# Kernel optimization log

Hardware: AMD Instinct MI355X
Metric: run time of the kernel (lower is better)

The kernel has to match this reference:

```python
import jax, jax.numpy as jnp
import numpy as np

N = 100000   # num_nodes
E = 1600000  # num_edges
R = 8        # num_rels
B = 4        # num_bases
D = 64       # inp_dim = h_dim = out_dim


def setup_inputs() -> dict:
    key = jax.random.key(0)
    ks = jax.random.split(key, 16)
    s = 1.0 / np.sqrt(D)
    inp = {
        'h': jax.random.normal(ks[0], (N, D), jnp.float32),
        'src': jax.random.randint(ks[1], (E,), 0, N),
        'dst': jax.random.randint(ks[2], (E,), 0, N),
        'etype': jax.random.randint(ks[3], (E,), 0, R),
        'norm': jax.random.uniform(ks[4], (E, 1), jnp.float32),
    }
    for i in range(3):  # i2h, hidden, h2o layers (basis decomposition)
        inp[f'bases{i}'] = jax.random.normal(ks[5 + 2 * i], (B, D, D), jnp.float32) * s
        inp[f'wcomp{i}'] = jax.random.normal(ks[6 + 2 * i], (R, B), jnp.float32) * s
    inp['dec_w1'] = jax.random.normal(ks[11], (D, D), jnp.float32) * s
    inp['dec_b1'] = jnp.zeros((D,), jnp.float32)
    inp['dec_w2'] = jax.random.normal(ks[12], (D, 1), jnp.float32) * s
    inp['dec_b2'] = jnp.zeros((1,), jnp.float32)
    return inp


def rgcn_layer(h, src, dst, etype, norm, bases, wcomp, activate):
    # basis decomposition: W_r = sum_b wcomp[r,b] * bases[b]
    W = jnp.einsum('rb,bio->rio', wcomp, bases)           # [R, D, D]
    # transform all nodes under every relation (dense GEMM), then gather per edge
    Ht = jnp.einsum('ni,rio->rno', h, W).reshape(R * N, -1)  # [R*N, D]
    msg = Ht[etype * N + src] * norm                      # [E, D] gather + norm
    out = jax.ops.segment_sum(msg, dst, num_segments=N)   # scatter-add to dst
    return jax.nn.relu(out) if activate else out


def reference(h, src, dst, etype, norm, bases0, wcomp0, bases1, wcomp1,
              bases2, wcomp2, dec_w1, dec_b1, dec_w2, dec_b2):
    # EncoderRGCN: i2h (relu) -> hidden (relu) -> h2o (no activation)
    h1 = rgcn_layer(h, src, dst, etype, norm, bases0, wcomp0, True)
    h2 = rgcn_layer(h1, src, dst, etype, norm, bases1, wcomp1, True)
    henc = rgcn_layer(h2, src, dst, etype, norm, bases2, wcomp2, False)
    # AttributeDecoder: Linear -> ReLU -> Linear(reconstruct_dim=1)
    d1 = jax.nn.relu(henc @ dec_w1 + dec_b1)
    rec = (d1 @ dec_w2 + dec_b2).squeeze()                # [N]
    return rec, henc
```

## Files before the change

kernel.cpp:

```cpp
#include <hip/hip_runtime.h>

typedef _Float16 half8 __attribute__((ext_vector_type(8)));
typedef _Float16 half4 __attribute__((ext_vector_type(4)));
typedef _Float16 half2v __attribute__((ext_vector_type(2)));
typedef float floatx4 __attribute__((ext_vector_type(4)));

constexpr int NN = 100000;
constexpr int EE = 1600000;
constexpr int NBK = 196;
constexpr int CHUNK = 6250;
constexpr int CAPB = 12288;
constexpr int NDCAP = 40;

__global__ __launch_bounds__(256) void k_part(const int* __restrict__ dst,
                                              const int* __restrict__ src,
                                              const int* __restrict__ etype,
                                              const float* __restrict__ norm,
                                              int* __restrict__ gcur,
                                              int2* __restrict__ part) {
  __shared__ int2 ldata[CHUNK];
  __shared__ unsigned char lbkt[CHUNK];
  __shared__ int lhist[NBK], lbase[NBK + 1], lcur[NBK], gbase[NBK];
  __shared__ int sh[256];
  const int tid = threadIdx.x;
  const int e0 = blockIdx.x * CHUNK;

  for (int b = tid; b < NBK; b += 256) lhist[b] = 0;
  __syncthreads();
  for (int i = tid; i < CHUNK; i += 256)
    atomicAdd(&lhist[dst[e0 + i] >> 9], 1);
  __syncthreads();
  {
    const int v = (tid < NBK) ? lhist[tid] : 0;
    sh[tid] = v;
    __syncthreads();
    int run = v;
    for (int d = 1; d < 256; d <<= 1) {
      int t = (tid >= d) ? sh[tid - d] : 0;
      __syncthreads();
      run += t;
      sh[tid] = run;
      __syncthreads();
    }
    if (tid < NBK) {
      lbase[tid] = run - v;
      lcur[tid] = 0;
      gbase[tid] = tid * CAPB + atomicAdd(&gcur[tid], v);
    }
    if (tid == 0) lbase[NBK] = CHUNK;
  }
  __syncthreads();
  for (int i = tid; i < CHUNK; i += 256) {
    const int e = e0 + i;
    const int d = dst[e], s = src[e], et = etype[e];
    const _Float16 nh = (_Float16)norm[e];
    const unsigned short n16 = __builtin_bit_cast(unsigned short, nh);
    const int bk = d >> 9;
    const int pos = lbase[bk] + atomicAdd(&lcur[bk], 1);
    ldata[pos] = make_int2((d << 15) | (s >> 2), (s & 3) | (et << 2) | ((int)n16 << 5));
    lbkt[pos] = (unsigned char)bk;
  }
  __syncthreads();
  for (int i = tid; i < CHUNK; i += 256) {
    const int bk = (int)lbkt[i];
    part[gbase[bk] + (i - lbase[bk])] = ldata[i];
  }
}

__global__ __launch_bounds__(256) void k_scanB(const int* __restrict__ gcur,
                                               int* __restrict__ ebase) {
  __shared__ int wsum[4];
  const int tid = threadIdx.x;
  const int v = (tid < NBK) ? gcur[tid] : 0;
  int incl = v;
  for (int d = 1; d < 64; d <<= 1) {
    const int t = __shfl_up(incl, d);
    if ((tid & 63) >= d) incl += t;
  }
  if ((tid & 63) == 63) wsum[tid >> 6] = incl;
  __syncthreads();
  int add = 0;
  for (int w = 0; w < (tid >> 6); ++w) add += wsum[w];
  incl += add;
  if (tid < NBK) ebase[tid] = incl - v;
  if (tid == NBK - 1) ebase[NBK] = incl;
}

__global__ __launch_bounds__(256) void k_part2(const int* __restrict__ gcur,
                                               const int* __restrict__ ebase,
                                               const int2* __restrict__ part,
                                               int* __restrict__ off,
                                               int2* __restrict__ em) {
  __shared__ int hcnt[512];
  __shared__ int obase[512];
  __shared__ int sh[256];
  const int tid = threadIdx.x;
  const int bk = blockIdx.x;
  const int nb0 = bk << 9;
  const int cntb = gcur[bk];
  const int base = ebase[bk];
  const int2* __restrict__ pp = part + (size_t)bk * CAPB;

  hcnt[tid] = 0;
  hcnt[tid + 256] = 0;
  __syncthreads();
  for (int i = tid; i < cntb; i += 256)
    atomicAdd(&hcnt[(((unsigned)pp[i].x) >> 15) & 511], 1);
  __syncthreads();
  const int c0 = hcnt[2 * tid], c1 = hcnt[2 * tid + 1];
  const int psum = c0 + c1;
  sh[tid] = psum;
  __syncthreads();
  int run = psum;
  for (int d = 1; d < 256; d <<= 1) {
    int t = (tid >= d) ? sh[tid - d] : 0;
    __syncthreads();
    run += t;
    sh[tid] = run;
    __syncthreads();
  }
  const int excl = run - psum;
  obase[2 * tid] = excl;
  obase[2 * tid + 1] = excl + c0;
  __syncthreads();
  {
    const int n = nb0 + tid;
    if (n < NN) off[n] = base + obase[tid];
    const int n2 = nb0 + 256 + tid;
    if (n2 < NN) off[n2] = base + obase[256 + tid];
  }
  if (bk == NBK - 1 && tid == 0) off[NN] = EE;
  hcnt[tid] = obase[tid];
  hcnt[tid + 256] = obase[tid + 256];
  __syncthreads();
  for (int i = tid; i < cntb; i += 256) {
    const int2 r = pp[i];
    const int d = ((unsigned)r.x) >> 15;
    const int s = ((r.x & 0x7FFF) << 2) | (r.y & 3);
    const int et = (r.y >> 2) & 7;
    const unsigned short n16 = (unsigned short)((r.y >> 5) & 0xFFFF);
    const float nf = (float)__builtin_bit_cast(_Float16, n16);
    const int pos = atomicAdd(&hcnt[d & 511], 1);
    em[base + pos] = make_int2((et << 20) | s, __float_as_int(nf));
  }
}


__global__ __launch_bounds__(256) void k_prep(const float* __restrict__ h,
                                              _Float16* __restrict__ hh,
                                              const float* __restrict__ b0,
                                              const float* __restrict__ b1,
                                              const float* __restrict__ b2,
                                              _Float16* __restrict__ bbt) {
  const int bx = blockIdx.x;
  if (bx < 6250) {
    const int i = bx * 256 + threadIdx.x;
    const float4 v = *(const float4*)&h[(size_t)i * 4];
    half4 o = {(_Float16)v.x, (_Float16)v.y, (_Float16)v.z, (_Float16)v.w};
    *(half4*)&hh[(size_t)i * 4] = o;
  } else {
    const int g = (bx - 6250) >> 6;
    const int idx = ((bx - 6250) & 63) * 256 + threadIdx.x;
    const float* bases = (g == 0) ? b0 : (g == 1) ? b1 : b2;
    const int o = idx >> 8, k = idx & 255;
    const int b = k >> 6, i = k & 63;
    bbt[g * 16384 + idx] = (_Float16)bases[b * 4096 + i * 64 + o];
  }
}

__global__ __launch_bounds__(256, 8) void k_layer(const _Float16* __restrict__ hh,
                                                  const int* __restrict__ off,
                                                  const int2* __restrict__ em,
                                                  const float* __restrict__ wcomp,
                                                  const _Float16* __restrict__ bbt,
                                                  _Float16* __restrict__ out16,
                                                  float* __restrict__ out32) {
  __shared__ _Float16 Ash[16 * 264];
  __shared__ int4 ems[16 * NDCAP];
  __shared__ float4 wcs[8];
  __shared__ int offs[17];
  __shared__ int ovf;
  const int tid = threadIdx.x;
  const int lane = tid & 63;
  const int wv = tid >> 6;
  const int n0 = blockIdx.x * 16;

  if (tid < 17) offs[tid] = off[n0 + tid];
  if (tid == 0) ovf = 0;
  if (tid < 8) wcs[tid] = ((const float4*)wcomp)[tid];
  for (int i = tid; i < 16 * NDCAP; i += 256) ems[i] = make_int4(0, 0, 0, 0);
  __syncthreads();

  const int e0 = offs[0];
  const int len = offs[16] - e0;
  for (int i = tid; i < len; i += 256) {
    const int g = e0 + i;
    const int2 r = em[g];
    int lo = 0, hi = 15;
    while (lo < hi) { const int mid = (lo + hi + 1) >> 1; if (offs[mid] <= g) lo = mid; else hi = mid - 1; }
    const int rank = g - offs[lo];
    const int et = r.x >> 20;
    const int s = r.x & 0xFFFFF;
    const float nf = __int_as_float(r.y);
    const float4 w = wcs[et];
    half2v c01 = {(_Float16)(nf * w.x), (_Float16)(nf * w.y)};
    half2v c23 = {(_Float16)(nf * w.z), (_Float16)(nf * w.w)};
    if (rank < NDCAP)
      ems[lo * NDCAP + rank] = make_int4(s, __builtin_bit_cast(int, c01),
                                         __builtin_bit_cast(int, c23), 0);
    else ovf = 1;
  }
  __syncthreads();

  if (!ovf) {
    const int fl = lane & 31;
    const int eg = lane >> 5;
    const half2v* __restrict__ hp = (const half2v*)hh;
    for (int q = 0; q < 4; ++q) {
      const int m = wv * 4 + q;
      const int cnt = offs[m + 1] - offs[m];
      const int nbat = (cnt + 7) >> 3;
      const int4* ep = &ems[m * NDCAP + eg * 4];
      float a0 = 0.f, a1 = 0.f, a2 = 0.f, a3 = 0.f;
      float a4 = 0.f, a5 = 0.f, a6 = 0.f, a7 = 0.f;
      for (int b = 0; b < nbat; ++b) {
        int4 rr[4];
#pragma unroll
        for (int j = 0; j < 4; ++j) rr[j] = ep[b * 8 + j];
        half2v hv[4];
#pragma unroll
        for (int j = 0; j < 4; ++j)
          hv[j] = hp[(unsigned)rr[j].x * 32u + fl];
#pragma unroll
        for (int j = 0; j < 4; ++j) {
          const half2v c01 = __builtin_bit_cast(half2v, rr[j].y);
          const half2v c23 = __builtin_bit_cast(half2v, rr[j].z);
          const float h0 = (float)hv[j][0], h1 = (float)hv[j][1];
          a0 = fmaf(h0, (float)c01[0], a0); a1 = fmaf(h1, (float)c01[0], a1);
          a2 = fmaf(h0, (float)c01[1], a2); a3 = fmaf(h1, (float)c01[1], a3);
          a4 = fmaf(h0, (float)c23[0], a4); a5 = fmaf(h1, (float)c23[0], a5);
          a6 = fmaf(h0, (float)c23[1], a6); a7 = fmaf(h1, (float)c23[1], a7);
        }
      }
      a0 += __shfl_xor(a0, 32); a1 += __shfl_xor(a1, 32);
      a2 += __shfl_xor(a2, 32); a3 += __shfl_xor(a3, 32);
      a4 += __shfl_xor(a4, 32); a5 += __shfl_xor(a5, 32);
      a6 += __shfl_xor(a6, 32); a7 += __shfl_xor(a7, 32);
      if (eg == 0) {
        _Float16* ar = &Ash[m * 264];
        *(half2v*)&ar[0 * 64 + 2 * fl] = half2v{(_Float16)a0, (_Float16)a1};
        *(half2v*)&ar[1 * 64 + 2 * fl] = half2v{(_Float16)a2, (_Float16)a3};
        *(half2v*)&ar[2 * 64 + 2 * fl] = half2v{(_Float16)a4, (_Float16)a5};
        *(half2v*)&ar[3 * 64 + 2 * fl] = half2v{(_Float16)a6, (_Float16)a7};
      }
    }
  } else {
    const _Float16* hl = hh + lane;
    for (int q = 0; q < 4; ++q) {
      const int m = wv * 4 + q;
      const int p0 = offs[m], p1 = offs[m + 1];
      float a0 = 0.f, a1 = 0.f, a2 = 0.f, a3 = 0.f;
      for (int p = p0; p < p1; p += 8) {
#pragma unroll
        for (int j = 0; j < 8; ++j) {
          const bool live = (p + j < p1);
          const int idx = live ? p + j : p1 - 1;
          const int2 mm = em[idx];
          const float hv = (float)hl[(size_t)(mm.x & 0xFFFFF) << 6];
          const float wn = live ? __int_as_float(mm.y) : 0.f;
          const float4 w = wcs[mm.x >> 20];
          const float t = wn * hv;
          a0 = fmaf(t, w.x, a0); a1 = fmaf(t, w.y, a1);
          a2 = fmaf(t, w.z, a2); a3 = fmaf(t, w.w, a3);
        }
      }
      _Float16* ar = &Ash[m * 264];
      ar[lane]       = (_Float16)a0;
      ar[64 + lane]  = (_Float16)a1;
      ar[128 + lane] = (_Float16)a2;
      ar[192 + lane] = (_Float16)a3;
    }
  }
  __syncthreads();

  const int col = lane & 15;
  const int quad = lane >> 4;
  const int obase = wv * 16 + col;
  const _Float16* ap = &Ash[col * 264 + quad * 8];
  const _Float16* bp = &bbt[(size_t)obase * 256 + quad * 8];
  floatx4 acc = {0.f, 0.f, 0.f, 0.f};
#pragma unroll
  for (int s = 0; s < 8; ++s) {
    const half8 af = *(const half8*)(ap + s * 32);
    const half8 bf = *(const half8*)(bp + s * 32);
    acc = __builtin_amdgcn_mfma_f32_16x16x32_f16(af, bf, acc, 0, 0, 0);
  }
  if (out16) {
#pragma unroll
    for (int r = 0; r < 4; ++r) {
      const float c = fmaxf(acc[r], 0.f);
      out16[(size_t)(n0 + quad * 4 + r) * 64 + obase] = (_Float16)c;
    }
  } else {
#pragma unroll
    for (int r = 0; r < 4; ++r) {
      out32[(size_t)(n0 + quad * 4 + r) * 64 + obase] = acc[r];
    }
  }
}

__global__ __launch_bounds__(256) void k_dec(const float* __restrict__ henc,
                                             const float* __restrict__ w1,
                                             const float* __restrict__ b1,
                                             const float* __restrict__ w2,
                                             const float* __restrict__ b2,
                                             float* __restrict__ rec) {
  __shared__ float w1s[64 * 64];
  __shared__ float hs[16 * 68];
  const int tid = threadIdx.x;
  for (int r = tid; r < 1024; r += 256)
    *(float4*)&w1s[r * 4] = *(const float4*)&w1[r * 4];
  const int og = tid & 15;
  const int nl = tid >> 4;
  const float4 wv2 = *(const float4*)&w2[og * 4];
  const float4 bv1 = *(const float4*)&b1[og * 4];
  const float b2v = b2[0];
  for (int t0 = blockIdx.x * 16; t0 < NN; t0 += gridDim.x * 16) {
    __syncthreads();
    {
      const float4 hv = *(const float4*)&henc[(size_t)t0 * 64 + tid * 4];
      *(float4*)&hs[(tid >> 4) * 68 + (tid & 15) * 4] = hv;
    }
    __syncthreads();
    float4 acc = bv1;
    const float* hr = &hs[nl * 68];
#pragma unroll 8
    for (int i = 0; i < 64; ++i) {
      const float hv = hr[i];
      const float4 wv = *(const float4*)&w1s[i * 64 + og * 4];
      acc.x = fmaf(hv, wv.x, acc.x); acc.y = fmaf(hv, wv.y, acc.y);
      acc.z = fmaf(hv, wv.z, acc.z); acc.w = fmaf(hv, wv.w, acc.w);
    }
    acc.x = fmaxf(acc.x, 0.f); acc.y = fmaxf(acc.y, 0.f);
    acc.z = fmaxf(acc.z, 0.f); acc.w = fmaxf(acc.w, 0.f);
    float v = acc.x * wv2.x + acc.y * wv2.y + acc.z * wv2.z + acc.w * wv2.w;
    v += __shfl_xor(v, 1); v += __shfl_xor(v, 2);
    v += __shfl_xor(v, 4); v += __shfl_xor(v, 8);
    if (og == 0) rec[t0 + nl] = v + b2v;
  }
}


extern "C" void kernel_launch(void* const* d_in, const int* in_sizes, int n_in,
                              void* d_out, int out_size, void* d_ws, size_t ws_size,
                              hipStream_t stream) {
  const float* h     = (const float*)d_in[0];
  const int*   src   = (const int*)d_in[1];
  const int*   dst   = (const int*)d_in[2];
  const int*   etype = (const int*)d_in[3];
  const float* norm  = (const float*)d_in[4];
  const float* bases[3] = {(const float*)d_in[5], (const float*)d_in[7], (const float*)d_in[9]};
  const float* wcomp[3] = {(const float*)d_in[6], (const float*)d_in[8], (const float*)d_in[10]};
  const float* dw1 = (const float*)d_in[11];
  const float* db1 = (const float*)d_in[12];
  const float* dw2 = (const float*)d_in[13];
  const float* db2 = (const float*)d_in[14];

  float* rec  = (float*)d_out;
  float* henc = (float*)d_out + NN;

  char* ws = (char*)d_ws;
  int*      off    = (int*)(ws + 0);
  int*      gcur   = (int*)(ws + 400512);
  int*      ebase  = (int*)(ws + 401536);
  int2*     em     = (int2*)(ws + 402560);
  _Float16* hh     = (_Float16*)(ws + 13202560);
  _Float16* h1f    = (_Float16*)(ws + 26002560);
  _Float16* h2f    = (_Float16*)(ws + 38802560);
  _Float16* bbt    = (_Float16*)(ws + 51602560);
  int2*     part   = (int2*)h1f;

  k_prep<<<6250 + 192, 256, 0, stream>>>(h, hh, bases[0], bases[1], bases[2], bbt);

  hipMemsetAsync(gcur, 0, NBK * sizeof(int), stream);
  k_part<<<256, 256, 0, stream>>>(dst, src, etype, norm, gcur, part);
  k_scanB<<<1, 256, 0, stream>>>(gcur, ebase);
  k_part2<<<NBK, 256, 0, stream>>>(gcur, ebase, part, off, em);

  k_layer<<<NN / 16, 256, 0, stream>>>(hh,  off, em, wcomp[0], bbt,         h1f, nullptr);
  k_layer<<<NN / 16, 256, 0, stream>>>(h1f, off, em, wcomp[1], bbt + 16384, h2f, nullptr);
  k_layer<<<NN / 16, 256, 0, stream>>>(h2f, off, em, wcomp[2], bbt + 32768, nullptr, henc);

  k_dec<<<256, 256, 0, stream>>>(henc, dw1, db1, dw2, db2, rec);
}
```

Measured before the change: 379.7 us.

## Pack fp16 aggregation, merge bucket scan into part2, fold memset into prep

The per-edge aggregation in the layer kernel now accumulates in packed half2 arithmetic, with source indices and broadcast coefficient pairs held in separate shared arrays and 8 edges per batch. The bucket-offset scan kernel is removed: each part2 block reduces the preceding bucket counts itself and uses 512 threads for its in-bucket scan. The gcur memset moves into the prep kernel, and partitioning uses smaller chunks across more blocks. NDCAP is raised and the occupancy hint lowered. Accumulating in fp16 cuts ALU work and conversions but risks precision loss, and the larger shared memory footprint may reduce occupancy.

Result: faster. 360.5 us (-5.1%).

```diff
diff --git a/kernel.cpp b/kernel.cpp
--- a/kernel.cpp
+++ b/kernel.cpp
@@ -8,9 +8,9 @@
 constexpr int NN = 100000;
 constexpr int EE = 1600000;
 constexpr int NBK = 196;
-constexpr int CHUNK = 6250;
+constexpr int CHUNK = 3125;
 constexpr int CAPB = 12288;
-constexpr int NDCAP = 40;
+constexpr int NDCAP = 48;
 
 __global__ __launch_bounds__(256) void k_part(const int* __restrict__ dst,
                                               const int* __restrict__ src,
@@ -67,73 +67,52 @@
   }
 }
 
-__global__ __launch_bounds__(256) void k_scanB(const int* __restrict__ gcur,
-                                               int* __restrict__ ebase) {
-  __shared__ int wsum[4];
+__global__ __launch_bounds__(512) void k_part2(const int* __restrict__ gcur,
+                                               const int2* __restrict__ part,
+                                               int* __restrict__ off,
+                                               int2* __restrict__ em) {
+  __shared__ int hcnt[512];
+  __shared__ int wred[8];
+  __shared__ int swsum[8];
   const int tid = threadIdx.x;
-  const int v = (tid < NBK) ? gcur[tid] : 0;
+  const int bk = blockIdx.x;
+  const int nb0 = bk << 9;
+  const int2* __restrict__ pp = part + (size_t)bk * CAPB;
+
+  {
+    int pv = (tid < bk) ? gcur[tid] : 0;
+    for (int d = 32; d > 0; d >>= 1) pv += __shfl_down(pv, d);
+    if ((tid & 63) == 0) wred[tid >> 6] = pv;
+  }
+  hcnt[tid] = 0;
+  __syncthreads();
+  int base = 0;
+#pragma unroll
+  for (int w = 0; w < 8; ++w) base += wred[w];
+  const int cntb = gcur[bk];
+
+  for (int i = tid; i < cntb; i += 512)
+    atomicAdd(&hcnt[(((unsigned)pp[i].x) >> 15) & 511], 1);
+  __syncthreads();
+  const int v = hcnt[tid];
   int incl = v;
   for (int d = 1; d < 64; d <<= 1) {
     const int t = __shfl_up(incl, d);
     if ((tid & 63) >= d) incl += t;
   }
-  if ((tid & 63) == 63) wsum[tid >> 6] = incl;
-  __syncthreads();
-  int add = 0;
-  for (int w = 0; w < (tid >> 6); ++w) add += wsum[w];
-  incl += add;
-  if (tid < NBK) ebase[tid] = incl - v;
-  if (tid == NBK - 1) ebase[NBK] = incl;
-}
-
-__global__ __launch_bounds__(256) void k_part2(const int* __restrict__ gcur,
-                                               const int* __restrict__ ebase,
-                                               const int2* __restrict__ part,
-                                               int* __restrict__ off,
-                                               int2* __restrict__ em) {
-  __shared__ int hcnt[512];
-  __shared__ int obase[512];
-  __shared__ int sh[256];
-  const int tid = threadIdx.x;
-  const int bk = blockIdx.x;
-  const int nb0 = bk << 9;
-  const int cntb = gcur[bk];
-  const int base = ebase[bk];
-  const int2* __restrict__ pp = part + (size_t)bk * CAPB;
-
-  hcnt[tid] = 0;
-  hcnt[tid + 256] = 0;
-  __syncthreads();
-  for (int i = tid; i < cntb; i += 256)
-    atomicAdd(&hcnt[(((unsigned)pp[i].x) >> 15) & 511], 1);
-  __syncthreads();
-  const int c0 = hcnt[2 * tid], c1 = hcnt[2 * tid + 1];
-  const int psum = c0 + c1;
-  sh[tid] = psum;
-  __syncthreads();
-  int run = psum;
-  for (int d = 1; d < 256; d <<= 1) {
-    int t = (tid >= d) ? sh[tid - d] : 0;
-    __syncthreads();
-    run += t;
-    sh[tid] = run;
-    __syncthreads();
-  }
-  const int excl = run - psum;
-  obase[2 * tid] = excl;
-  obase[2 * tid + 1] = excl + c0;
-  __syncthreads();
+  if ((tid & 63) == 63) swsum[tid >> 6] = incl;
+  __syncthreads();
+  int pre = 0;
+  for (int w = 0; w < (tid >> 6); ++w) pre += swsum[w];
+  const int excl = pre + incl - v;
   {
     const int n = nb0 + tid;
-    if (n < NN) off[n] = base + obase[tid];
-    const int n2 = nb0 + 256 + tid;
-    if (n2 < NN) off[n2] = base + obase[256 + tid];
+    if (n < NN) off[n] = base + excl;
   }
   if (bk == NBK - 1 && tid == 0) off[NN] = EE;
-  hcnt[tid] = obase[tid];
-  hcnt[tid + 256] = obase[tid + 256];
-  __syncthreads();
-  for (int i = tid; i < cntb; i += 256) {
+  hcnt[tid] = excl;
+  __syncthreads();
+  for (int i = tid; i < cntb; i += 512) {
     const int2 r = pp[i];
     const int d = ((unsigned)r.x) >> 15;
     const int s = ((r.x & 0x7FFF) << 2) | (r.y & 3);
@@ -151,8 +130,10 @@
                                               const float* __restrict__ b0,
                                               const float* __restrict__ b1,
                                               const float* __restrict__ b2,
-                                              _Float16* __restrict__ bbt) {
+                                              _Float16* __restrict__ bbt,
+                                              int* __restrict__ gcur) {
   const int bx = blockIdx.x;
+  if (bx == 0 && threadIdx.x < NBK) gcur[threadIdx.x] = 0;
   if (bx < 6250) {
     const int i = bx * 256 + threadIdx.x;
     const float4 v = *(const float4*)&h[(size_t)i * 4];
@@ -168,7 +149,7 @@
   }
 }
 
-__global__ __launch_bounds__(256, 8) void k_layer(const _Float16* __restrict__ hh,
+__global__ __launch_bounds__(256, 6) void k_layer(const _Float16* __restrict__ hh,
                                                   const int* __restrict__ off,
                                                   const int2* __restrict__ em,
                                                   const float* __restrict__ wcomp,
@@ -176,7 +157,8 @@
                                                   _Float16* __restrict__ out16,
                                                   float* __restrict__ out32) {
   __shared__ _Float16 Ash[16 * 264];
-  __shared__ int4 ems[16 * NDCAP];
+  __shared__ int  ems_s[16 * NDCAP];
+  __shared__ int4 ems_c[16 * NDCAP];
   __shared__ float4 wcs[8];
   __shared__ int offs[17];
   __shared__ int ovf;
@@ -188,7 +170,10 @@
   if (tid < 17) offs[tid] = off[n0 + tid];
   if (tid == 0) ovf = 0;
   if (tid < 8) wcs[tid] = ((const float4*)wcomp)[tid];
-  for (int i = tid; i < 16 * NDCAP; i += 256) ems[i] = make_int4(0, 0, 0, 0);
+  for (int i = tid; i < 16 * NDCAP; i += 256) {
+    ems_s[i] = 0;
+    ems_c[i] = make_int4(0, 0, 0, 0);
+  }
   __syncthreads();
 
   const int e0 = offs[0];
@@ -203,12 +188,15 @@
     const int s = r.x & 0xFFFFF;
     const float nf = __int_as_float(r.y);
     const float4 w = wcs[et];
-    half2v c01 = {(_Float16)(nf * w.x), (_Float16)(nf * w.y)};
-    half2v c23 = {(_Float16)(nf * w.z), (_Float16)(nf * w.w)};
-    if (rank < NDCAP)
-      ems[lo * NDCAP + rank] = make_int4(s, __builtin_bit_cast(int, c01),
-                                         __builtin_bit_cast(int, c23), 0);
-    else ovf = 1;
+    const _Float16 c0 = (_Float16)(nf * w.x), c1 = (_Float16)(nf * w.y);
+    const _Float16 c2 = (_Float16)(nf * w.z), c3 = (_Float16)(nf * w.w);
+    const half2v p0 = {c0, c0}, p1 = {c1, c1}, p2 = {c2, c2}, p3 = {c3, c3};
+    if (rank < NDCAP) {
+      ems_s[lo * NDCAP + rank] = s;
+      ems_c[lo * NDCAP + rank] = make_int4(
+          __builtin_bit_cast(int, p0), __builtin_bit_cast(int, p1),
+          __builtin_bit_cast(int, p2), __builtin_bit_cast(int, p3));
+    } else ovf = 1;
   }
   __syncthreads();
 
@@ -219,39 +207,37 @@
     for (int q = 0; q < 4; ++q) {
       const int m = wv * 4 + q;
       const int cnt = offs[m + 1] - offs[m];
-      const int nbat = (cnt + 7) >> 3;
-      const int4* ep = &ems[m * NDCAP + eg * 4];
-      float a0 = 0.f, a1 = 0.f, a2 = 0.f, a3 = 0.f;
-      float a4 = 0.f, a5 = 0.f, a6 = 0.f, a7 = 0.f;
+      const int nbat = (cnt + 15) >> 4;
+      const int* sp = &ems_s[m * NDCAP + eg * 8];
+      const int4* cp = &ems_c[m * NDCAP + eg * 8];
+      half2v a0 = {0, 0}, a1 = {0, 0}, a2 = {0, 0}, a3 = {0, 0};
       for (int b = 0; b < nbat; ++b) {
-        int4 rr[4];
-#pragma unroll
-        for (int j = 0; j < 4; ++j) rr[j] = ep[b * 8 + j];
-        half2v hv[4];
-#pragma unroll
-        for (int j = 0; j < 4; ++j)
-          hv[j] = hp[(unsigned)rr[j].x * 32u + fl];
-#pragma unroll
-        for (int j = 0; j < 4; ++j) {
-          const half2v c01 = __builtin_bit_cast(half2v, rr[j].y);
-          const half2v c23 = __builtin_bit_cast(half2v, rr[j].z);
-          const float h0 = (float)hv[j][0], h1 = (float)hv[j][1];
-          a0 = fmaf(h0, (float)c01[0], a0); a1 = fmaf(h1, (float)c01[0], a1);
-          a2 = fmaf(h0, (float)c01[1], a2); a3 = fmaf(h1, (float)c01[1], a3);
-          a4 = fmaf(h0, (float)c23[0], a4); a5 = fmaf(h1, (float)c23[0], a5);
-          a6 = fmaf(h0, (float)c23[1], a6); a7 = fmaf(h1, (float)c23[1], a7);
+        int s8[8];
+#pragma unroll
+        for (int j = 0; j < 8; ++j) s8[j] = sp[b * 16 + j];
+        half2v hv[8];
+#pragma unroll
+        for (int j = 0; j < 8; ++j)
+          hv[j] = hp[(unsigned)s8[j] * 32u + fl];
+#pragma unroll
+        for (int j = 0; j < 8; ++j) {
+          const int4 cc = cp[b * 16 + j];
+          a0 = a0 + hv[j] * __builtin_bit_cast(half2v, cc.x);
+          a1 = a1 + hv[j] * __builtin_bit_cast(half2v, cc.y);
+          a2 = a2 + hv[j] * __builtin_bit_cast(half2v, cc.z);
+          a3 = a3 + hv[j] * __builtin_bit_cast(half2v, cc.w);
         }
       }
-      a0 += __shfl_xor(a0, 32); a1 += __shfl_xor(a1, 32);
-      a2 += __shfl_xor(a2, 32); a3 += __shfl_xor(a3, 32);
-      a4 += __shfl_xor(a4, 32); a5 += __shfl_xor(a5, 32);
-      a6 += __shfl_xor(a6, 32); a7 += __shfl_xor(a7, 32);
+      a0 = a0 + __builtin_bit_cast(half2v, __shfl_xor(__builtin_bit_cast(int, a0), 32));
+      a1 = a1 + __builtin_bit_cast(half2v, __shfl_xor(__builtin_bit_cast(int, a1), 32));
+      a2 = a2 + __builtin_bit_cast(half2v, __shfl_xor(__builtin_bit_cast(int, a2), 32));
+      a3 = a3 + __builtin_bit_cast(half2v, __shfl_xor(__builtin_bit_cast(int, a3), 32));
       if (eg == 0) {
         _Float16* ar = &Ash[m * 264];
-        *(half2v*)&ar[0 * 64 + 2 * fl] = half2v{(_Float16)a0, (_Float16)a1};
-        *(half2v*)&ar[1 * 64 + 2 * fl] = half2v{(_Float16)a2, (_Float16)a3};
-        *(half2v*)&ar[2 * 64 + 2 * fl] = half2v{(_Float16)a4, (_Float16)a5};
-        *(half2v*)&ar[3 * 64 + 2 * fl] = half2v{(_Float16)a6, (_Float16)a7};
+        *(half2v*)&ar[0 * 64 + 2 * fl] = a0;
+        *(half2v*)&ar[1 * 64 + 2 * fl] = a1;
+        *(half2v*)&ar[2 * 64 + 2 * fl] = a2;
+        *(half2v*)&ar[3 * 64 + 2 * fl] = a3;
       }
     }
   } else {
@@ -372,7 +358,6 @@
   char* ws = (char*)d_ws;
   int*      off    = (int*)(ws + 0);
   int*      gcur   = (int*)(ws + 400512);
-  int*      ebase  = (int*)(ws + 401536);
   int2*     em     = (int2*)(ws + 402560);
   _Float16* hh     = (_Float16*)(ws + 13202560);
   _Float16* h1f    = (_Float16*)(ws + 26002560);
@@ -380,12 +365,10 @@
   _Float16* bbt    = (_Float16*)(ws + 51602560);
   int2*     part   = (int2*)h1f;
 
-  k_prep<<<6250 + 192, 256, 0, stream>>>(h, hh, bases[0], bases[1], bases[2], bbt);
-
-  hipMemsetAsync(gcur, 0, NBK * sizeof(int), stream);
-  k_part<<<256, 256, 0, stream>>>(dst, src, etype, norm, gcur, part);
-  k_scanB<<<1, 256, 0, stream>>>(gcur, ebase);
-  k_part2<<<NBK, 256, 0, stream>>>(gcur, ebase, part, off, em);
+  k_prep<<<6250 + 192, 256, 0, stream>>>(h, hh, bases[0], bases[1], bases[2], bbt, gcur);
+
+  k_part<<<512, 256, 0, stream>>>(dst, src, etype, norm, gcur, part);
+  k_part2<<<NBK, 512, 0, stream>>>(gcur, part, off, em);
 
   k_layer<<<NN / 16, 256, 0, stream>>>(hh,  off, em, wcomp[0], bbt,         h1f, nullptr);
   k_layer<<<NN / 16, 256, 0, stream>>>(h1f, off, em, wcomp[1], bbt + 16384, h2f, nullptr);
```
